# Optimization experiments

Measured on AMD Instinct MI355X. Metric: run time of the kernel, lower is better.

The kernel has to match this reference:

```python
import jax, jax.numpy as jnp
import numpy as np

B, C_IN, C_HID, C_OUT, T = 32, 512, 512, 256, 4096


def setup_inputs() -> dict:
    key = jax.random.key(0)
    k_x, k_w1, k_b1, k_w2, k_b2 = jax.random.split(key, 5)
    x = jax.random.normal(k_x, (B, C_IN, T), dtype=jnp.float32)
    # small init scale ~ 1/sqrt(fan_in) to keep activations/softmax well-behaved
    W1 = jax.random.normal(k_w1, (C_HID, C_IN), dtype=jnp.float32) * (1.0 / np.sqrt(C_IN))
    b1 = jax.random.normal(k_b1, (C_HID,), dtype=jnp.float32) * 0.01
    W2 = jax.random.normal(k_w2, (C_OUT, C_HID), dtype=jnp.float32) * (1.0 / np.sqrt(C_HID))
    b2 = jax.random.normal(k_b2, (C_OUT,), dtype=jnp.float32) * 0.01
    return {"x": x, "W1": W1, "b1": b1, "W2": W2, "b2": b2}


def reference(x, W1, b1, W2, b2):
    # Conv1x1 (kernel_size=1) == per-timestep matmul over channels: 'oi,bit->bot'
    h = jax.nn.relu(jnp.einsum('oi,bit->bot', W1, x) + b1[None, :, None])  # [B, C_HID, T]
    y = jnp.einsum('oi,bit->bot', W2, h) + b2[None, :, None]               # [B, C_OUT, T]
    last = y[:, :, -1]                                                     # Sample(): [B, C_OUT]
    # nn.Softmax() on 2D input -> softmax over dim=1
    return jax.nn.softmax(last, axis=1)
```

## Files before the change

kernel.cpp:

```cpp
#include <hip/hip_runtime.h>
#include <hip/hip_bf16.h>
#include <math.h>

#define BB   32
#define CIN  512
#define CHID 512
#define COUT 256
#define TT   4096

__global__ __launch_bounds__(512) void mlp_last_softmax(
    const float* __restrict__ x,
    const float* __restrict__ W1,
    const float* __restrict__ b1,
    const float* __restrict__ W2,
    const float* __restrict__ b2,
    float* __restrict__ out)
{
    __shared__ float xv[CIN];
    __shared__ float h[CHID];
    __shared__ float ys[COUT];
    __shared__ float redmax[8];
    __shared__ float redsum[8];

    const int b = blockIdx.x;
    const int t = threadIdx.x;

    xv[t] = x[(size_t)b * ((size_t)CIN * TT) + (size_t)t * TT + (TT - 1)];
    __syncthreads();

    {
        const float4* wr  = reinterpret_cast<const float4*>(W1 + (size_t)t * CIN);
        const float4* xv4 = reinterpret_cast<const float4*>(xv);
        float a0 = 0.f, a1 = 0.f, a2 = 0.f, a3 = 0.f;
        #pragma unroll
        for (int i = 0; i < CIN / 4; i += 4) {
            float4 w0 = wr[i],    w1 = wr[i + 1],  w2 = wr[i + 2],  w3 = wr[i + 3];
            float4 v0 = xv4[i],   v1 = xv4[i + 1], v2 = xv4[i + 2], v3 = xv4[i + 3];
            a0 += w0.x * v0.x + w0.y * v0.y + w0.z * v0.z + w0.w * v0.w;
            a1 += w1.x * v1.x + w1.y * v1.y + w1.z * v1.z + w1.w * v1.w;
            a2 += w2.x * v2.x + w2.y * v2.y + w2.z * v2.z + w2.w * v2.w;
            a3 += w3.x * v3.x + w3.y * v3.y + w3.z * v3.z + w3.w * v3.w;
        }
        float s = (a0 + a1) + (a2 + a3) + b1[t];
        h[t] = fmaxf(s, 0.f);
    }
    __syncthreads();

    {
        const int o    = t >> 1;
        const int half = t & 1;
        const float4* wr = reinterpret_cast<const float4*>(W2 + (size_t)o * CHID + half * (CHID / 2));
        const float4* h4 = reinterpret_cast<const float4*>(h) + half * (CHID / 8);
        float a0 = 0.f, a1 = 0.f;
        #pragma unroll
        for (int i = 0; i < CHID / 8; i += 2) {
            float4 w0 = wr[i], w1 = wr[i + 1];
            float4 v0 = h4[i], v1 = h4[i + 1];
            a0 += w0.x * v0.x + w0.y * v0.y + w0.z * v0.z + w0.w * v0.w;
            a1 += w1.x * v1.x + w1.y * v1.y + w1.z * v1.z + w1.w * v1.w;
        }
        float acc = a0 + a1;
        acc += __shfl_xor(acc, 1);
        if (half == 0) ys[o] = acc + b2[o];
    }
    __syncthreads();

    const int wid  = t >> 6;
    const int lane = t & 63;

    float val = (t < COUT) ? ys[t] : -INFINITY;
    float m = val;
    #pragma unroll
    for (int s = 1; s < 64; s <<= 1) m = fmaxf(m, __shfl_xor(m, s));
    if (lane == 0) redmax[wid] = m;
    __syncthreads();
    float mall = redmax[0];
    #pragma unroll
    for (int i = 1; i < 8; ++i) mall = fmaxf(mall, redmax[i]);

    float e = (t < COUT) ? expf(val - mall) : 0.f;
    float ssum = e;
    #pragma unroll
    for (int s = 1; s < 64; s <<= 1) ssum += __shfl_xor(ssum, s);
    if (lane == 0) redsum[wid] = ssum;
    __syncthreads();
    float tot = 0.f;
    #pragma unroll
    for (int i = 0; i < 8; ++i) tot += redsum[i];

    if (t < COUT) out[(size_t)b * COUT + t] = e / tot;
}

extern "C" void kernel_launch(void* const* d_in, const int* in_sizes, int n_in,
                              void* d_out, int out_size, void* d_ws, size_t ws_size,
                              hipStream_t stream) {
    const float* x  = (const float*)d_in[0];
    const float* W1 = (const float*)d_in[1];
    const float* b1 = (const float*)d_in[2];
    const float* W2 = (const float*)d_in[3];
    const float* b2 = (const float*)d_in[4];
    float* out = (float*)d_out;

    mlp_last_softmax<<<BB, 512, 0, stream>>>(x, W1, b1, W2, b2, out);
}
```

Measured before the change: 354.6 us.

## Split hidden layer into a separate wide-grid kernel to raise parallelism

Splits the single 32-block kernel in two. The first kernel computes the hidden layer across a 32x8 grid, with four threads per row and coalesced W1 reads, and writes to a workspace. The second kernel computes the output layer and softmax. The fused version used only 32 blocks on a GPU with many CUs, and each thread read its own W1 row with strided access. The split adds a kernel launch and a workspace round trip, and every hidden block redundantly gathers the strided x column.

```diff
diff --git a/kernel.cpp b/kernel.cpp
--- a/kernel.cpp
+++ b/kernel.cpp
@@ -8,15 +8,53 @@
 #define COUT 256
 #define TT   4096
 
-__global__ __launch_bounds__(512) void mlp_last_softmax(
+
+__global__ __launch_bounds__(256) void k1_hidden(
     const float* __restrict__ x,
     const float* __restrict__ W1,
     const float* __restrict__ b1,
+    float* __restrict__ hws)
+{
+    __shared__ float xv[CIN];
+
+    const int b   = blockIdx.x;
+    const int s   = blockIdx.y;
+    const int tid = threadIdx.x;
+
+    const size_t xbase = (size_t)b * ((size_t)CIN * TT) + (TT - 1);
+    xv[tid]       = x[xbase + (size_t)tid * TT];
+    xv[tid + 256] = x[xbase + (size_t)(tid + 256) * TT];
+    __syncthreads();
+
+    const int rl = tid >> 2;
+    const int q  = tid & 3;
+    const int r  = s * 64 + rl;
+
+    const float4* wr = reinterpret_cast<const float4*>(W1 + (size_t)r * CIN) + q * 32;
+    const float4* xp = reinterpret_cast<const float4*>(xv) + q * 32;
+
+    float a0 = 0.f, a1 = 0.f, a2 = 0.f, a3 = 0.f;
+    #pragma unroll
+    for (int i = 0; i < 32; i += 4) {
+        float4 w0 = wr[i],   w1 = wr[i+1], w2 = wr[i+2], w3 = wr[i+3];
+        float4 v0 = xp[i],   v1 = xp[i+1], v2 = xp[i+2], v3 = xp[i+3];
+        a0 += w0.x*v0.x + w0.y*v0.y + w0.z*v0.z + w0.w*v0.w;
+        a1 += w1.x*v1.x + w1.y*v1.y + w1.z*v1.z + w1.w*v1.w;
+        a2 += w2.x*v2.x + w2.y*v2.y + w2.z*v2.z + w2.w*v2.w;
+        a3 += w3.x*v3.x + w3.y*v3.y + w3.z*v3.z + w3.w*v3.w;
+    }
+    float acc = (a0 + a1) + (a2 + a3);
+    acc += __shfl_xor(acc, 1);
+    acc += __shfl_xor(acc, 2);
+    if (q == 0) hws[b * CHID + r] = fmaxf(acc + b1[r], 0.f);
+}
+
+__global__ __launch_bounds__(512) void k2_out_softmax(
+    const float* __restrict__ hws,
     const float* __restrict__ W2,
     const float* __restrict__ b2,
     float* __restrict__ out)
 {
-    __shared__ float xv[CIN];
     __shared__ float h[CHID];
     __shared__ float ys[COUT];
     __shared__ float redmax[8];
@@ -25,25 +63,7 @@
     const int b = blockIdx.x;
     const int t = threadIdx.x;
 
-    xv[t] = x[(size_t)b * ((size_t)CIN * TT) + (size_t)t * TT + (TT - 1)];
-    __syncthreads();
-
-    {
-        const float4* wr  = reinterpret_cast<const float4*>(W1 + (size_t)t * CIN);
-        const float4* xv4 = reinterpret_cast<const float4*>(xv);
-        float a0 = 0.f, a1 = 0.f, a2 = 0.f, a3 = 0.f;
-        #pragma unroll
-        for (int i = 0; i < CIN / 4; i += 4) {
-            float4 w0 = wr[i],    w1 = wr[i + 1],  w2 = wr[i + 2],  w3 = wr[i + 3];
-            float4 v0 = xv4[i],   v1 = xv4[i + 1], v2 = xv4[i + 2], v3 = xv4[i + 3];
-            a0 += w0.x * v0.x + w0.y * v0.y + w0.z * v0.z + w0.w * v0.w;
-            a1 += w1.x * v1.x + w1.y * v1.y + w1.z * v1.z + w1.w * v1.w;
-            a2 += w2.x * v2.x + w2.y * v2.y + w2.z * v2.z + w2.w * v2.w;
-            a3 += w3.x * v3.x + w3.y * v3.y + w3.z * v3.z + w3.w * v3.w;
-        }
-        float s = (a0 + a1) + (a2 + a3) + b1[t];
-        h[t] = fmaxf(s, 0.f);
-    }
+    h[t] = hws[b * CHID + t];
     __syncthreads();
 
     {
@@ -56,8 +76,8 @@
         for (int i = 0; i < CHID / 8; i += 2) {
             float4 w0 = wr[i], w1 = wr[i + 1];
             float4 v0 = h4[i], v1 = h4[i + 1];
-            a0 += w0.x * v0.x + w0.y * v0.y + w0.z * v0.z + w0.w * v0.w;
-            a1 += w1.x * v1.x + w1.y * v1.y + w1.z * v1.z + w1.w * v1.w;
+            a0 += w0.x*v0.x + w0.y*v0.y + w0.z*v0.z + w0.w*v0.w;
+            a1 += w1.x*v1.x + w1.y*v1.y + w1.z*v1.z + w1.w*v1.w;
         }
         float acc = a0 + a1;
         acc += __shfl_xor(acc, 1);
@@ -100,6 +120,8 @@
     const float* W2 = (const float*)d_in[3];
     const float* b2 = (const float*)d_in[4];
     float* out = (float*)d_out;
+    float* hws = (float*)d_ws;
 
-    mlp_last_softmax<<<BB, 512, 0, stream>>>(x, W1, b1, W2, b2, out);
+    k1_hidden<<<dim3(BB, 8), 256, 0, stream>>>(x, W1, b1, hws);
+    k2_out_softmax<<<BB, 512, 0, stream>>>(hws, W2, b2, out);
 }
```

Result: faster. 321.9 us (-9.2%).
